# Performance work log

Hardware: AMD Instinct MI355X
Metric: run time of the kernel (lower is better)

The kernel has to match this reference:

```python
import jax, jax.numpy as jnp
import numpy as np

N_NODES = 100000
N_EDGES = 1600000
NUM_GRAPHS = 128
IN_F = 32
K = 3  # TAGConv default number of hops


def setup_inputs() -> dict:
    key = jax.random.key(0)
    ks = jax.random.split(key, 12)
    x = jax.random.normal(ks[0], (N_NODES, IN_F), dtype=jnp.float32)
    edge_index = jax.random.randint(ks[1], (2, N_EDGES), 0, N_NODES, dtype=jnp.int32)
    batch = jnp.sort(jax.random.randint(ks[2], (N_NODES,), 0, NUM_GRAPHS, dtype=jnp.int32))
    edge_weight = jax.random.uniform(ks[3], (N_EDGES,), dtype=jnp.float32)
    # TAGConv params: K+1 weight matrices per layer (bias shared per layer)
    s1 = 1.0 / np.sqrt(IN_F)
    s2 = 1.0 / np.sqrt(8)
    s3 = 1.0 / np.sqrt(32)
    W1 = jax.random.uniform(ks[4], (K + 1, IN_F, 8), jnp.float32, -s1, s1)
    b1 = jax.random.uniform(ks[5], (8,), jnp.float32, -s1, s1)
    W2 = jax.random.uniform(ks[6], (K + 1, 8, 16), jnp.float32, -s2, s2)
    b2 = jax.random.uniform(ks[7], (16,), jnp.float32, -s2, s2)
    Wfc = jax.random.uniform(ks[8], (32, 2), jnp.float32, -s3, s3)
    bfc = jax.random.uniform(ks[9], (2,), jnp.float32, -s3, s3)
    return {"x": x, "edge_index": edge_index, "batch": batch, "edge_weight": edge_weight,
            "W1": W1, "b1": b1, "W2": W2, "b2": b2, "Wfc": Wfc, "bfc": bfc}


def reference(x, edge_index, batch, edge_weight, W1, b1, W2, b2, Wfc, bfc):
    src, dst = edge_index[0], edge_index[1]
    n = x.shape[0]
    # gcn_norm without self-loops (TAGConv default): D^-1/2 A D^-1/2
    deg = jax.ops.segment_sum(edge_weight, dst, num_segments=n)
    dinv = jnp.where(deg > 0, jax.lax.rsqrt(jnp.maximum(deg, 1e-30)), 0.0)
    norm = dinv[src] * edge_weight * dinv[dst]

    def tag_conv(h, W, b):
        out = h @ W[0]
        for k in range(1, W.shape[0]):
            # sparse propagate: gather at src, scale, scatter-add at dst
            h = jax.ops.segment_sum(h[src] * norm[:, None], dst, num_segments=n)
            out = out + h @ W[k]
        return out + b

    h = jax.nn.relu(tag_conv(x, W1, b1))
    h = jax.nn.relu(tag_conv(h, W2, b2))
    # global max pool + global mean pool over graphs in the batch
    mx = jax.ops.segment_max(h, batch, num_segments=NUM_GRAPHS)
    cnt = jax.ops.segment_sum(jnp.ones((n,), h.dtype), batch, num_segments=NUM_GRAPHS)
    mean = jax.ops.segment_sum(h, batch, num_segments=NUM_GRAPHS) / jnp.maximum(cnt, 1.0)[:, None]
    return jnp.concatenate([mx, mean], axis=1) @ Wfc + bfc
```

## Files before the change

kernel.cpp:

```cpp
#include <hip/hip_runtime.h>

constexpr int NN = 100000;
constexpr int NE = 1600000;
constexpr int NG = 128;

constexpr int SCAN_T = 256;
constexpr int SCAN_B = (NN + SCAN_T - 1) / SCAN_T;

struct __align__(8) Ent { int s; float nw; };


__global__ void k_rank(const int4* __restrict__ dst4, int* __restrict__ cnt,
                       ushort4* __restrict__ rank4, int ne4) {
    int i = blockIdx.x * blockDim.x + threadIdx.x;
    if (i >= ne4) return;
    int4 d = dst4[i];
    ushort4 r;
    r.x = (ushort)atomicAdd(&cnt[d.x], 1);
    r.y = (ushort)atomicAdd(&cnt[d.y], 1);
    r.z = (ushort)atomicAdd(&cnt[d.z], 1);
    r.w = (ushort)atomicAdd(&cnt[d.w], 1);
    rank4[i] = r;
}

__global__ void k_scan1b(const int* __restrict__ cnt, int* __restrict__ bsum,
                         const int* __restrict__ batch, int* __restrict__ gstart, int nn) {
    __shared__ int s[SCAN_T];
    int b = blockIdx.x;
    if (b < SCAN_B) {
        int i = b * SCAN_T + threadIdx.x;
        s[threadIdx.x] = (i < nn) ? ((cnt[i] + 1) & ~1) : 0;
        __syncthreads();
        for (int off = SCAN_T / 2; off > 0; off >>= 1) {
            if (threadIdx.x < off) s[threadIdx.x] += s[threadIdx.x + off];
            __syncthreads();
        }
        if (threadIdx.x == 0) bsum[b] = s[0];
    } else {
        int i = (b - SCAN_B) * SCAN_T + threadIdx.x;
        if (i >= nn) return;
        int bb = batch[i];
        int prev = (i == 0) ? -1 : batch[i - 1];
        for (int g = prev + 1; g <= bb; ++g) gstart[g] = i;
        if (i == nn - 1) {
            for (int g = bb + 1; g <= NG; ++g) gstart[g] = nn;
        }
    }
}

__global__ void k_scan2(int* __restrict__ bsum, int nb) {
    __shared__ int s[512];
    int t = threadIdx.x;
    s[t] = (t < nb) ? bsum[t] : 0;
    __syncthreads();
    for (int off = 1; off < 512; off <<= 1) {
        int v = (t >= off) ? s[t - off] : 0;
        __syncthreads();
        s[t] += v;
        __syncthreads();
    }
    if (t < nb) bsum[t] = (t > 0) ? s[t - 1] : 0;
}

__global__ void k_scan3(const int* __restrict__ cnt, const int* __restrict__ bsum,
                        int* __restrict__ row_ptr, Ent* __restrict__ csr, int nn) {
    __shared__ int s[SCAN_T];
    int t = threadIdx.x;
    int i = blockIdx.x * SCAN_T + t;
    int c0 = (i < nn) ? cnt[i] : 0;
    int v = (c0 + 1) & ~1;
    s[t] = v;
    __syncthreads();
    for (int off = 1; off < SCAN_T; off <<= 1) {
        int u = (t >= off) ? s[t - off] : 0;
        __syncthreads();
        s[t] += u;
        __syncthreads();
    }
    int incl = s[t];
    int base = bsum[blockIdx.x];
    if (i < nn) {
        int rp = base + incl - v;
        row_ptr[i] = rp;
        if (i == nn - 1) row_ptr[nn] = base + incl;
        if (c0 & 1) {
            Ent z; z.s = 0; z.nw = 0.f;
            csr[rp + c0] = z;
        }
    }
}

__global__ void k_scatter2(const int4* __restrict__ src4, const int4* __restrict__ dst4,
                           const float4* __restrict__ w4, const int* __restrict__ row_ptr,
                           const ushort4* __restrict__ rank4, Ent* __restrict__ csr, int ne4) {
    int i = blockIdx.x * blockDim.x + threadIdx.x;
    if (i >= ne4) return;
    int4 s = src4[i]; int4 d = dst4[i]; float4 w = w4[i]; ushort4 r = rank4[i];
    Ent e0; e0.s = s.x; e0.nw = w.x; csr[row_ptr[d.x] + r.x] = e0;
    Ent e1; e1.s = s.y; e1.nw = w.y; csr[row_ptr[d.y] + r.y] = e1;
    Ent e2; e2.s = s.z; e2.nw = w.z; csr[row_ptr[d.z] + r.z] = e2;
    Ent e3; e3.s = s.w; e3.nw = w.w; csr[row_ptr[d.w] + r.w] = e3;
}

__global__ void k_degi(const int* __restrict__ row_ptr, const float4* __restrict__ csr4,
                       float* __restrict__ dinv, int nn) {
    int tid = blockIdx.x * blockDim.x + threadIdx.x;
    int n = tid >> 3, lane = tid & 7;
    if (n >= nn) return;
    int beg = row_ptr[n] >> 1, end = row_ptr[n + 1] >> 1;
    float s = 0.f;
    for (int p = beg + lane; p < end; p += 8) {
        float4 a = csr4[p];
        s += a.y + a.w;
    }
    s += __shfl_xor(s, 1, 64);
    s += __shfl_xor(s, 2, 64);
    s += __shfl_xor(s, 4, 64);
    if (lane == 0) dinv[n] = s > 0.f ? rsqrtf(fmaxf(s, 1e-30f)) : 0.f;
}

__global__ void k_mm4(const float* __restrict__ h, const float* __restrict__ W,
                      const float* __restrict__ dinv, float* __restrict__ t, int nn) {
    __shared__ float sW[4 * 32 * 8];
    for (int i = threadIdx.x; i < 4 * 32 * 8; i += blockDim.x) sW[i] = W[i];
    __syncthreads();
    int n = blockIdx.x * blockDim.x + threadIdx.x;
    if (n >= nn) return;
    float hr[32];
    const float4* hp = reinterpret_cast<const float4*>(h + (size_t)n * 32);
#pragma unroll
    for (int f = 0; f < 8; ++f) {
        float4 v = hp[f];
        hr[4 * f + 0] = v.x; hr[4 * f + 1] = v.y;
        hr[4 * f + 2] = v.z; hr[4 * f + 3] = v.w;
    }
    float dv = dinv[n];
#pragma unroll
    for (int k = 0; k < 4; ++k) {
        float acc[8];
#pragma unroll
        for (int j = 0; j < 8; ++j) acc[j] = 0.f;
#pragma unroll
        for (int i = 0; i < 32; ++i) {
            float hv = hr[i];
            const float* wrow = &sW[(k * 32 + i) * 8];
#pragma unroll
            for (int j = 0; j < 8; ++j) acc[j] = fmaf(hv, wrow[j], acc[j]);
        }
        if (k == 3) {
#pragma unroll
            for (int j = 0; j < 8; ++j) acc[j] *= dv;
        }
        float4* op = reinterpret_cast<float4*>(t + ((size_t)k * nn + n) * 8);
        op[0] = make_float4(acc[0], acc[1], acc[2], acc[3]);
        op[1] = make_float4(acc[4], acc[5], acc[6], acc[7]);
    }
}

__global__ void k_pull8(const int* __restrict__ row_ptr, const float4* __restrict__ csr4,
                        const float* __restrict__ dinv,
                        const float* __restrict__ hin, const float* __restrict__ add,
                        float* __restrict__ hout, int nn) {
    constexpr int F = 8;
    int g = blockIdx.x * (blockDim.x / F) + threadIdx.x / F;
    int lane = threadIdx.x & (F - 1);
    if (g >= nn) return;
    int p = row_ptr[g] >> 1, end = row_ptr[g + 1] >> 1;
    float acc0 = 0.f, acc1 = 0.f, acc2 = 0.f, acc3 = 0.f;
    for (; p + 2 <= end; p += 2) {
        float4 a = csr4[p], c = csr4[p + 1];
        acc0 = fmaf(hin[(size_t)__float_as_int(a.x) * F + lane], a.y, acc0);
        acc1 = fmaf(hin[(size_t)__float_as_int(a.z) * F + lane], a.w, acc1);
        acc2 = fmaf(hin[(size_t)__float_as_int(c.x) * F + lane], c.y, acc2);
        acc3 = fmaf(hin[(size_t)__float_as_int(c.z) * F + lane], c.w, acc3);
    }
    if (p < end) {
        float4 a = csr4[p];
        acc0 = fmaf(hin[(size_t)__float_as_int(a.x) * F + lane], a.y, acc0);
        acc1 = fmaf(hin[(size_t)__float_as_int(a.z) * F + lane], a.w, acc1);
    }
    float acc = (acc0 + acc1) + (acc2 + acc3);
    float dv = dinv[g];
    hout[(size_t)g * F + lane] = dv * (dv * acc + add[(size_t)g * F + lane]);
}

__global__ void k_pull8_final(const int* __restrict__ row_ptr, const float4* __restrict__ csr4,
                              const float* __restrict__ dinv,
                              const float* __restrict__ hin, const float* __restrict__ add,
                              const float* __restrict__ b1, const float* __restrict__ W23,
                              float* __restrict__ h1, float* __restrict__ U3, int nn) {
    __shared__ float sW[8 * 16];
    if (threadIdx.x < 128) sW[threadIdx.x] = W23[threadIdx.x];
    __syncthreads();
    constexpr int F = 8;
    int g = blockIdx.x * (blockDim.x / F) + threadIdx.x / F;
    int lane = threadIdx.x & (F - 1);
    if (g >= nn) return;
    int p = row_ptr[g] >> 1, end = row_ptr[g + 1] >> 1;
    float acc0 = 0.f, acc1 = 0.f, acc2 = 0.f, acc3 = 0.f;
    for (; p + 2 <= end; p += 2) {
        float4 a = csr4[p], c = csr4[p + 1];
        acc0 = fmaf(hin[(size_t)__float_as_int(a.x) * F + lane], a.y, acc0);
        acc1 = fmaf(hin[(size_t)__float_as_int(a.z) * F + lane], a.w, acc1);
        acc2 = fmaf(hin[(size_t)__float_as_int(c.x) * F + lane], c.y, acc2);
        acc3 = fmaf(hin[(size_t)__float_as_int(c.z) * F + lane], c.w, acc3);
    }
    if (p < end) {
        float4 a = csr4[p];
        acc0 = fmaf(hin[(size_t)__float_as_int(a.x) * F + lane], a.y, acc0);
        acc1 = fmaf(hin[(size_t)__float_as_int(a.z) * F + lane], a.w, acc1);
    }
    float acc = (acc0 + acc1) + (acc2 + acc3);
    float dv = dinv[g];
    float r = fmaxf(dv * acc + add[(size_t)g * F + lane] + b1[lane], 0.f);
    h1[(size_t)g * F + lane] = r;
    float u0 = 0.f, u1 = 0.f;
#pragma unroll
    for (int i = 0; i < 8; ++i) {
        float hv = __shfl(r, i, 8);
        u0 = fmaf(hv, sW[i * 16 + lane], u0);
        u1 = fmaf(hv, sW[i * 16 + lane + 8], u1);
    }
    U3[(size_t)g * 16 + lane] = dv * u0;
    U3[(size_t)g * 16 + lane + 8] = dv * u1;
}

template <bool FINAL>
__global__ void k_pullW(const int* __restrict__ row_ptr, const float4* __restrict__ csr4,
                        const float* __restrict__ dinv,
                        const float* __restrict__ hin, const float* __restrict__ h1,
                        const float* __restrict__ W2k, const float* __restrict__ b2,
                        float* __restrict__ hout, int nn) {
    __shared__ float sW[8 * 16];
    if (threadIdx.x < 128) sW[threadIdx.x] = W2k[threadIdx.x];
    __syncthreads();
    constexpr int F = 16;
    int g = blockIdx.x * (blockDim.x / F) + threadIdx.x / F;
    int lane = threadIdx.x & (F - 1);
    if (g >= nn) return;
    int p = row_ptr[g] >> 1, end = row_ptr[g + 1] >> 1;
    float acc0 = 0.f, acc1 = 0.f, acc2 = 0.f, acc3 = 0.f;
    for (; p + 2 <= end; p += 2) {
        float4 a = csr4[p], c = csr4[p + 1];
        acc0 = fmaf(hin[(size_t)__float_as_int(a.x) * F + lane], a.y, acc0);
        acc1 = fmaf(hin[(size_t)__float_as_int(a.z) * F + lane], a.w, acc1);
        acc2 = fmaf(hin[(size_t)__float_as_int(c.x) * F + lane], c.y, acc2);
        acc3 = fmaf(hin[(size_t)__float_as_int(c.z) * F + lane], c.w, acc3);
    }
    if (p < end) {
        float4 a = csr4[p];
        acc0 = fmaf(hin[(size_t)__float_as_int(a.x) * F + lane], a.y, acc0);
        acc1 = fmaf(hin[(size_t)__float_as_int(a.z) * F + lane], a.w, acc1);
    }
    float acc = (acc0 + acc1) + (acc2 + acc3);
    const float4* h1p = reinterpret_cast<const float4*>(h1 + (size_t)g * 8);
    float4 ha = h1p[0], hb = h1p[1];
    float add = ha.x * sW[0 * 16 + lane];
    add = fmaf(ha.y, sW[1 * 16 + lane], add);
    add = fmaf(ha.z, sW[2 * 16 + lane], add);
    add = fmaf(ha.w, sW[3 * 16 + lane], add);
    add = fmaf(hb.x, sW[4 * 16 + lane], add);
    add = fmaf(hb.y, sW[5 * 16 + lane], add);
    add = fmaf(hb.z, sW[6 * 16 + lane], add);
    add = fmaf(hb.w, sW[7 * 16 + lane], add);
    float dv = dinv[g];
    float r;
    if (FINAL) r = fmaxf(dv * acc + add + b2[lane], 0.f);
    else       r = dv * (dv * acc + add);
    hout[(size_t)g * F + lane] = r;
}


__global__ void k_pool2(const float* __restrict__ h, const int* __restrict__ start,
                        const float* __restrict__ Wfc, const float* __restrict__ bfc,
                        float* __restrict__ out) {
    int g = blockIdx.x;
    int beg = start[g], end = start[g + 1];
    int tid = threadIdx.x;
    int feat = tid & 15, grp = tid >> 4;
    float mx = 0.f, sm = 0.f;
    for (int n = beg + grp; n < end; n += 16) {
        float v = h[(size_t)n * 16 + feat];
        mx = fmaxf(mx, v);
        sm += v;
    }
    mx = fmaxf(mx, __shfl_xor(mx, 16, 64));
    sm += __shfl_xor(sm, 16, 64);
    mx = fmaxf(mx, __shfl_xor(mx, 32, 64));
    sm += __shfl_xor(sm, 32, 64);
    __shared__ float smx[4][16], ssm[4][16];
    int wave = tid >> 6;
    int lane = tid & 63;
    if (lane < 16) { smx[wave][feat] = mx; ssm[wave][feat] = sm; }
    __syncthreads();
    if (tid < 16) {
        float m = fmaxf(fmaxf(smx[0][tid], smx[1][tid]), fmaxf(smx[2][tid], smx[3][tid]));
        float s = ssm[0][tid] + ssm[1][tid] + ssm[2][tid] + ssm[3][tid];
        smx[0][tid] = m;
        ssm[0][tid] = (end > beg) ? s / (float)(end - beg) : 0.f;
    }
    __syncthreads();
    if (tid < 2) {
        float acc = bfc[tid];
#pragma unroll
        for (int i = 0; i < 16; ++i) acc += smx[0][i] * Wfc[i * 2 + tid];
#pragma unroll
        for (int i = 0; i < 16; ++i) acc += ssm[0][i] * Wfc[(16 + i) * 2 + tid];
        out[g * 2 + tid] = acc;
    }
}


extern "C" void kernel_launch(void* const* d_in, const int* in_sizes, int n_in,
                              void* d_out, int out_size, void* d_ws, size_t ws_size,
                              hipStream_t stream) {
    const float* x    = (const float*)d_in[0];
    const int*   eidx = (const int*)d_in[1];
    const int*   srcp = eidx;
    const int*   dstp = eidx + NE;
    const int*   batch= (const int*)d_in[2];
    const float* ew   = (const float*)d_in[3];
    const float* W1   = (const float*)d_in[4];
    const float* b1   = (const float*)d_in[5];
    const float* W2   = (const float*)d_in[6];
    const float* b2   = (const float*)d_in[7];
    const float* Wfc  = (const float*)d_in[8];
    const float* bfc  = (const float*)d_in[9];
    float* out = (float*)d_out;

    constexpr size_t NN8  = (size_t)NN * 8;
    constexpr size_t NN16 = (size_t)NN * 16;

    float*  dinv    = (float*)d_ws;
    int*    cnt     = (int*)(dinv + NN);
    int*    row_ptr = cnt + NN;
    ushort* rank    = (ushort*)(row_ptr + NN + 4);
    Ent*    csr     = (Ent*)((int*)(void*)rank + NE / 2);
    float*  uni     = (float*)(csr + NE + NN);
    float*  h1      = uni + 4 * NN16;
    int*    gstart  = (int*)(h1 + NN8);
    int*    bsum    = gstart + NG + 4;

    float* T  = uni;
    float* P  = uni + 2 * NN16;
    float* P2 = P + NN8;
    float* U3   = uni + 3 * NN16;
    float* q    = uni + 0 * NN16;
    float* q2   = uni + 1 * NN16;
    float* out2 = uni + 2 * NN16;

    const float4* csr4 = (const float4*)csr;

    const int BLK = 256;
    const int NE4 = NE / 4;
    const int gE4 = (NE4 + BLK - 1) / BLK;
    const int gN  = (NN + BLK - 1) / BLK;
    const int gP8  = (NN + (BLK / 8) - 1) / (BLK / 8);
    const int gP16 = (NN + (BLK / 16) - 1) / (BLK / 16);
    const int gN8  = (NN * 8 + BLK - 1) / BLK;

    hipMemsetAsync(cnt, 0, (size_t)NN * sizeof(int), stream);
    k_rank<<<gE4, BLK, 0, stream>>>((const int4*)dstp, cnt, (ushort4*)rank, NE4);
    k_scan1b<<<SCAN_B + gN, SCAN_T, 0, stream>>>(cnt, bsum, batch, gstart, NN);
    k_scan2<<<1, 512, 0, stream>>>(bsum, SCAN_B);
    k_scan3<<<SCAN_B, SCAN_T, 0, stream>>>(cnt, bsum, row_ptr, csr, NN);
    k_scatter2<<<gE4, BLK, 0, stream>>>((const int4*)srcp, (const int4*)dstp,
                                        (const float4*)ew, row_ptr, (const ushort4*)rank,
                                        csr, NE4);
    k_degi<<<gN8, BLK, 0, stream>>>(row_ptr, csr4, dinv, NN);

    k_mm4<<<gN, BLK, 0, stream>>>(x, W1, dinv, T, NN);
    k_pull8<<<gP8, BLK, 0, stream>>>(row_ptr, csr4, dinv, T + 3 * NN8, T + 2 * NN8, P, NN);
    k_pull8<<<gP8, BLK, 0, stream>>>(row_ptr, csr4, dinv, P, T + 1 * NN8, P2, NN);
    k_pull8_final<<<gP8, BLK, 0, stream>>>(row_ptr, csr4, dinv, P2, T, b1,
                                           W2 + 3 * 128, h1, U3, NN);

    k_pullW<false><<<gP16, BLK, 0, stream>>>(row_ptr, csr4, dinv, U3, h1, W2 + 2 * 128, nullptr, q, NN);
    k_pullW<false><<<gP16, BLK, 0, stream>>>(row_ptr, csr4, dinv, q,  h1, W2 + 1 * 128, nullptr, q2, NN);
    k_pullW<true ><<<gP16, BLK, 0, stream>>>(row_ptr, csr4, dinv, q2, h1, W2 + 0 * 128, b2, out2, NN);

    k_pool2<<<NG, 256, 0, stream>>>(out2, gstart, Wfc, bfc, out);
}
```

Before: 297.4 us.

## Degree-sort nodes via binned permutation for balanced pull kernels; fuse scan kernels

Builds a permutation of nodes grouped by in-degree bin (counting sort using per-block histograms and global cursors), and makes the degree and all pull/propagate kernels process nodes in that order. The goal is to cut wave-level load imbalance when lanes in one wavefront handle nodes of very different degrees. It also merges the block-sum scan into k_scan3 (each block redundantly scans the block sums) and folds the histogram pass into the auxiliary kernel, which removes one launch. The cost is an extra perm indirection per node and scattered writes to node outputs, which lose the coalescing that sequential node order gave.

```diff
diff --git a/kernel.cpp b/kernel.cpp
--- a/kernel.cpp
+++ b/kernel.cpp
@@ -6,6 +6,8 @@
 
 constexpr int SCAN_T = 256;
 constexpr int SCAN_B = (NN + SCAN_T - 1) / SCAN_T;
+constexpr int G_N    = (NN + 255) / 256;
+constexpr int NBIN   = 128;
 
 struct __align__(8) Ent { int s; float nw; };
 
@@ -23,8 +25,9 @@
     rank4[i] = r;
 }
 
-__global__ void k_scan1b(const int* __restrict__ cnt, int* __restrict__ bsum,
-                         const int* __restrict__ batch, int* __restrict__ gstart, int nn) {
+__global__ void k_aux(const int* __restrict__ cnt, int* __restrict__ bsum,
+                      const int* __restrict__ batch, int* __restrict__ gstart,
+                      int* __restrict__ gbins, int nn) {
     __shared__ int s[SCAN_T];
     int b = blockIdx.x;
     if (b < SCAN_B) {
@@ -36,7 +39,7 @@
             __syncthreads();
         }
         if (threadIdx.x == 0) bsum[b] = s[0];
-    } else {
+    } else if (b < SCAN_B + G_N) {
         int i = (b - SCAN_B) * SCAN_T + threadIdx.x;
         if (i >= nn) return;
         int bb = batch[i];
@@ -45,49 +48,89 @@
         if (i == nn - 1) {
             for (int g = bb + 1; g <= NG; ++g) gstart[g] = nn;
         }
-    }
-}
-
-__global__ void k_scan2(int* __restrict__ bsum, int nb) {
-    __shared__ int s[512];
-    int t = threadIdx.x;
-    s[t] = (t < nb) ? bsum[t] : 0;
-    __syncthreads();
-    for (int off = 1; off < 512; off <<= 1) {
-        int v = (t >= off) ? s[t - off] : 0;
-        __syncthreads();
-        s[t] += v;
-        __syncthreads();
-    }
-    if (t < nb) bsum[t] = (t > 0) ? s[t - 1] : 0;
-}
-
-__global__ void k_scan3(const int* __restrict__ cnt, const int* __restrict__ bsum,
-                        int* __restrict__ row_ptr, Ent* __restrict__ csr, int nn) {
+    } else {
+        int t = threadIdx.x;
+        if (t < NBIN) s[t] = 0;
+        __syncthreads();
+        int i = (b - SCAN_B - G_N) * SCAN_T + t;
+        if (i < nn) {
+            int bin = min((cnt[i] + 1) >> 1, NBIN - 1);
+            atomicAdd(&s[bin], 1);
+        }
+        __syncthreads();
+        if (t < NBIN && s[t] > 0) atomicAdd(&gbins[t], s[t]);
+    }
+}
+
+__global__ void __launch_bounds__(512) k_scan3(const int* __restrict__ cnt,
+                                               const int* __restrict__ bsum,
+                                               int* __restrict__ row_ptr,
+                                               Ent* __restrict__ csr, int nn) {
+    __shared__ int sb[512];
     __shared__ int s[SCAN_T];
     int t = threadIdx.x;
+    sb[t] = (t < SCAN_B) ? bsum[t] : 0;
+    __syncthreads();
+    for (int off = 1; off < 512; off <<= 1) {
+        int v = (t >= off) ? sb[t - off] : 0;
+        __syncthreads();
+        sb[t] += v;
+        __syncthreads();
+    }
+    int base = (blockIdx.x > 0) ? sb[blockIdx.x - 1] : 0;
     int i = blockIdx.x * SCAN_T + t;
-    int c0 = (i < nn) ? cnt[i] : 0;
-    int v = (c0 + 1) & ~1;
-    s[t] = v;
+    int c0 = 0, v = 0;
+    if (t < SCAN_T) {
+        c0 = (i < nn) ? cnt[i] : 0;
+        v = (c0 + 1) & ~1;
+        s[t] = v;
+    }
     __syncthreads();
     for (int off = 1; off < SCAN_T; off <<= 1) {
-        int u = (t >= off) ? s[t - off] : 0;
-        __syncthreads();
-        s[t] += u;
-        __syncthreads();
-    }
-    int incl = s[t];
-    int base = bsum[blockIdx.x];
-    if (i < nn) {
-        int rp = base + incl - v;
+        int u = (t >= off && t < SCAN_T) ? s[t - off] : 0;
+        __syncthreads();
+        if (t < SCAN_T) s[t] += u;
+        __syncthreads();
+    }
+    if (t < SCAN_T && i < nn) {
+        int rp = base + s[t] - v;
         row_ptr[i] = rp;
-        if (i == nn - 1) row_ptr[nn] = base + incl;
+        if (i == nn - 1) row_ptr[nn] = base + s[t];
         if (c0 & 1) {
             Ent z; z.s = 0; z.nw = 0.f;
             csr[rp + c0] = z;
         }
     }
+}
+
+__global__ void k_perm(const int* __restrict__ cnt, const int* __restrict__ gbins,
+                       int* __restrict__ gcursor, int* __restrict__ perm, int nn) {
+    __shared__ int lcnt[NBIN], lrel[NBIN], lstart[NBIN], sb2[NBIN];
+    int t = threadIdx.x;
+    if (t < NBIN) lcnt[t] = 0;
+    __syncthreads();
+    int n = blockIdx.x * blockDim.x + t;
+    int bin = 0, myIdx = 0;
+    bool act = (n < nn);
+    if (act) {
+        bin = min((cnt[n] + 1) >> 1, NBIN - 1);
+        myIdx = atomicAdd(&lcnt[bin], 1);
+    }
+    __syncthreads();
+    if (t < NBIN) {
+        lrel[t] = lcnt[t] ? atomicAdd(&gcursor[t], lcnt[t]) : 0;
+        sb2[t] = gbins[t];
+    }
+    __syncthreads();
+    for (int off = 1; off < NBIN; off <<= 1) {
+        int v = (t >= off && t < NBIN) ? sb2[t - off] : 0;
+        __syncthreads();
+        if (t < NBIN) sb2[t] += v;
+        __syncthreads();
+    }
+    if (t < NBIN) lstart[t] = (t > 0) ? sb2[t - 1] : 0;
+    __syncthreads();
+    if (act) perm[lstart[bin] + lrel[bin] + myIdx] = n;
 }
 
 __global__ void k_scatter2(const int4* __restrict__ src4, const int4* __restrict__ dst4,
@@ -103,10 +146,11 @@
 }
 
 __global__ void k_degi(const int* __restrict__ row_ptr, const float4* __restrict__ csr4,
-                       float* __restrict__ dinv, int nn) {
+                       const int* __restrict__ perm, float* __restrict__ dinv, int nn) {
     int tid = blockIdx.x * blockDim.x + threadIdx.x;
-    int n = tid >> 3, lane = tid & 7;
-    if (n >= nn) return;
+    int gi = tid >> 3, lane = tid & 7;
+    if (gi >= nn) return;
+    int n = perm[gi];
     int beg = row_ptr[n] >> 1, end = row_ptr[n + 1] >> 1;
     float s = 0.f;
     for (int p = beg + lane; p < end; p += 8) {
@@ -158,13 +202,14 @@
 }
 
 __global__ void k_pull8(const int* __restrict__ row_ptr, const float4* __restrict__ csr4,
-                        const float* __restrict__ dinv,
+                        const int* __restrict__ perm, const float* __restrict__ dinv,
                         const float* __restrict__ hin, const float* __restrict__ add,
                         float* __restrict__ hout, int nn) {
     constexpr int F = 8;
-    int g = blockIdx.x * (blockDim.x / F) + threadIdx.x / F;
+    int gi = blockIdx.x * (blockDim.x / F) + threadIdx.x / F;
     int lane = threadIdx.x & (F - 1);
-    if (g >= nn) return;
+    if (gi >= nn) return;
+    int g = perm[gi];
     int p = row_ptr[g] >> 1, end = row_ptr[g + 1] >> 1;
     float acc0 = 0.f, acc1 = 0.f, acc2 = 0.f, acc3 = 0.f;
     for (; p + 2 <= end; p += 2) {
@@ -185,7 +230,7 @@
 }
 
 __global__ void k_pull8_final(const int* __restrict__ row_ptr, const float4* __restrict__ csr4,
-                              const float* __restrict__ dinv,
+                              const int* __restrict__ perm, const float* __restrict__ dinv,
                               const float* __restrict__ hin, const float* __restrict__ add,
                               const float* __restrict__ b1, const float* __restrict__ W23,
                               float* __restrict__ h1, float* __restrict__ U3, int nn) {
@@ -193,9 +238,10 @@
     if (threadIdx.x < 128) sW[threadIdx.x] = W23[threadIdx.x];
     __syncthreads();
     constexpr int F = 8;
-    int g = blockIdx.x * (blockDim.x / F) + threadIdx.x / F;
+    int gi = blockIdx.x * (blockDim.x / F) + threadIdx.x / F;
     int lane = threadIdx.x & (F - 1);
-    if (g >= nn) return;
+    if (gi >= nn) return;
+    int g = perm[gi];
     int p = row_ptr[g] >> 1, end = row_ptr[g + 1] >> 1;
     float acc0 = 0.f, acc1 = 0.f, acc2 = 0.f, acc3 = 0.f;
     for (; p + 2 <= end; p += 2) {
@@ -227,7 +273,7 @@
 
 template <bool FINAL>
 __global__ void k_pullW(const int* __restrict__ row_ptr, const float4* __restrict__ csr4,
-                        const float* __restrict__ dinv,
+                        const int* __restrict__ perm, const float* __restrict__ dinv,
                         const float* __restrict__ hin, const float* __restrict__ h1,
                         const float* __restrict__ W2k, const float* __restrict__ b2,
                         float* __restrict__ hout, int nn) {
@@ -235,9 +281,10 @@
     if (threadIdx.x < 128) sW[threadIdx.x] = W2k[threadIdx.x];
     __syncthreads();
     constexpr int F = 16;
-    int g = blockIdx.x * (blockDim.x / F) + threadIdx.x / F;
+    int gi = blockIdx.x * (blockDim.x / F) + threadIdx.x / F;
     int lane = threadIdx.x & (F - 1);
-    if (g >= nn) return;
+    if (gi >= nn) return;
+    int g = perm[gi];
     int p = row_ptr[g] >> 1, end = row_ptr[g + 1] >> 1;
     float acc0 = 0.f, acc1 = 0.f, acc2 = 0.f, acc3 = 0.f;
     for (; p + 2 <= end; p += 2) {
@@ -333,8 +380,11 @@
 
     float*  dinv    = (float*)d_ws;
     int*    cnt     = (int*)(dinv + NN);
-    int*    row_ptr = cnt + NN;
-    ushort* rank    = (ushort*)(row_ptr + NN + 4);
+    int*    gbins   = cnt + NN;
+    int*    gcursor = gbins + NBIN;
+    int*    row_ptr = gcursor + NBIN;
+    int*    perm    = row_ptr + NN + 4;
+    ushort* rank    = (ushort*)(perm + NN);
     Ent*    csr     = (Ent*)((int*)(void*)rank + NE / 2);
     float*  uni     = (float*)(csr + NE + NN);
     float*  h1      = uni + 4 * NN16;
@@ -359,25 +409,25 @@
     const int gP16 = (NN + (BLK / 16) - 1) / (BLK / 16);
     const int gN8  = (NN * 8 + BLK - 1) / BLK;
 
-    hipMemsetAsync(cnt, 0, (size_t)NN * sizeof(int), stream);
+    hipMemsetAsync(cnt, 0, (size_t)(NN + 2 * NBIN) * sizeof(int), stream);
     k_rank<<<gE4, BLK, 0, stream>>>((const int4*)dstp, cnt, (ushort4*)rank, NE4);
-    k_scan1b<<<SCAN_B + gN, SCAN_T, 0, stream>>>(cnt, bsum, batch, gstart, NN);
-    k_scan2<<<1, 512, 0, stream>>>(bsum, SCAN_B);
-    k_scan3<<<SCAN_B, SCAN_T, 0, stream>>>(cnt, bsum, row_ptr, csr, NN);
+    k_aux<<<SCAN_B + 2 * G_N, SCAN_T, 0, stream>>>(cnt, bsum, batch, gstart, gbins, NN);
+    k_scan3<<<SCAN_B, 512, 0, stream>>>(cnt, bsum, row_ptr, csr, NN);
+    k_perm<<<gN, BLK, 0, stream>>>(cnt, gbins, gcursor, perm, NN);
     k_scatter2<<<gE4, BLK, 0, stream>>>((const int4*)srcp, (const int4*)dstp,
                                         (const float4*)ew, row_ptr, (const ushort4*)rank,
                                         csr, NE4);
-    k_degi<<<gN8, BLK, 0, stream>>>(row_ptr, csr4, dinv, NN);
+    k_degi<<<gN8, BLK, 0, stream>>>(row_ptr, csr4, perm, dinv, NN);
 
     k_mm4<<<gN, BLK, 0, stream>>>(x, W1, dinv, T, NN);
-    k_pull8<<<gP8, BLK, 0, stream>>>(row_ptr, csr4, dinv, T + 3 * NN8, T + 2 * NN8, P, NN);
-    k_pull8<<<gP8, BLK, 0, stream>>>(row_ptr, csr4, dinv, P, T + 1 * NN8, P2, NN);
-    k_pull8_final<<<gP8, BLK, 0, stream>>>(row_ptr, csr4, dinv, P2, T, b1,
+    k_pull8<<<gP8, BLK, 0, stream>>>(row_ptr, csr4, perm, dinv, T + 3 * NN8, T + 2 * NN8, P, NN);
+    k_pull8<<<gP8, BLK, 0, stream>>>(row_ptr, csr4, perm, dinv, P, T + 1 * NN8, P2, NN);
+    k_pull8_final<<<gP8, BLK, 0, stream>>>(row_ptr, csr4, perm, dinv, P2, T, b1,
                                            W2 + 3 * 128, h1, U3, NN);
 
-    k_pullW<false><<<gP16, BLK, 0, stream>>>(row_ptr, csr4, dinv, U3, h1, W2 + 2 * 128, nullptr, q, NN);
-    k_pullW<false><<<gP16, BLK, 0, stream>>>(row_ptr, csr4, dinv, q,  h1, W2 + 1 * 128, nullptr, q2, NN);
-    k_pullW<true ><<<gP16, BLK, 0, stream>>>(row_ptr, csr4, dinv, q2, h1, W2 + 0 * 128, b2, out2, NN);
+    k_pullW<false><<<gP16, BLK, 0, stream>>>(row_ptr, csr4, perm, dinv, U3, h1, W2 + 2 * 128, nullptr, q, NN);
+    k_pullW<false><<<gP16, BLK, 0, stream>>>(row_ptr, csr4, perm, dinv, q,  h1, W2 + 1 * 128, nullptr, q2, NN);
+    k_pullW<true ><<<gP16, BLK, 0, stream>>>(row_ptr, csr4, perm, dinv, q2, h1, W2 + 0 * 128, b2, out2, NN);
 
     k_pool2<<<NG, 256, 0, stream>>>(out2, gstart, Wfc, bfc, out);
 }
```

After: 327.7 us. +10.2%, slower.
